# Kernel optimization log

Hardware: AMD Instinct MI355X
Metric: run time of the kernel (lower is better)

Reference implementation:

```python
import jax, jax.numpy as jnp
import numpy as np

B, C, H, W = 8, 512, 64, 64
S = 64
STD = 0.001  # torch init.normal_(weight, std=0.001)


def setup_inputs() -> dict:
    key = jax.random.key(0)
    ks = jax.random.split(key, 7)
    return {
        "queries": jax.random.normal(ks[0], (B, C, H, W), dtype=jnp.float32),
        "k": jax.random.normal(ks[1], (B, C, H, W), dtype=jnp.float32),
        "v": jax.random.normal(ks[2], (B, C, H, W), dtype=jnp.float32),
        "Wq": jax.random.normal(ks[3], (S, C), dtype=jnp.float32) * STD,
        "Wk": jax.random.normal(ks[4], (S, C), dtype=jnp.float32) * STD,
        "Wv": jax.random.normal(ks[5], (S, C), dtype=jnp.float32) * STD,
        "Wl": jax.random.normal(ks[6], (C, S), dtype=jnp.float32) * STD,
    }


def _branch(A, Bp, Cp, Wl):
    # A,Bp,Cp: [h,w,b,S] projected tensors
    m = jnp.einsum('hwbs,hwbt->hwst', A, Bp)          # [h,w,S,S]
    m = jax.nn.softmax(m, axis=1)                      # softmax over w (dim=1, as in torch)
    o = jnp.einsum('hwst,hwbt->hwsb', m, Cp)           # [h,w,S,b]
    o = o / jnp.sum(o, axis=2, keepdims=True)          # normalize over S
    o = jnp.einsum('hwsb,cs->hwbc', o, Wl)             # transpose + Linear(S->C)
    return jnp.transpose(o, (2, 3, 0, 1))              # [b,c,h,w]


def reference(queries, k, v, Wq, Wk, Wv, Wl):
    q = jnp.transpose(queries, (2, 3, 0, 1))  # [h,w,b,c]
    kk = jnp.transpose(k, (2, 3, 0, 1))
    vv = jnp.transpose(v, (2, 3, 0, 1))
    aq = jnp.einsum('hwbc,sc->hwbs', q, Wq)   # [h,w,b,S]
    ak = jnp.einsum('hwbc,sc->hwbs', kk, Wk)
    av = jnp.einsum('hwbc,sc->hwbs', vv, Wv)
    out_q = _branch(aq, ak, av, Wl)
    out_k = _branch(ak, av, aq, Wl)
    out_v = _branch(av, aq, ak, Wl)
    return jnp.concatenate((out_q, out_k, out_v), axis=0)  # [3b,c,h,w]
```

## Files before the change

### kernel.cpp

```cpp
#include <hip/hip_runtime.h>
#include <hip/hip_bf16.h>

#define HW 4096
#define CCH 512
#define SDIM 64
#define BDIM 8

typedef __attribute__((ext_vector_type(8))) short short8;
typedef __attribute__((ext_vector_type(4))) float f32x4;

static __device__ __forceinline__ ushort f2bf(float f) {
  __hip_bfloat16 h = __float2bfloat16(f);
  return *reinterpret_cast<ushort*>(&h);
}
static __device__ __forceinline__ float bf2f(ushort u) {
  union { unsigned int u32; float f; } c;
  c.u32 = ((unsigned int)u) << 16;
  return c.f;
}
static __device__ __forceinline__ ushort trunc_bf(float f, float* rem) {
  union { float f; unsigned int u; } a; a.f = f;
  union { float f; unsigned int u; } h; h.u = a.u & 0xFFFF0000u;
  *rem = f - h.f;
  return (ushort)(a.u >> 16);
}
static __device__ __forceinline__ ushort rne_bf(float f) {
  union { float f; unsigned int u; } a; a.f = f;
  return (ushort)((a.u + 0x8000u) >> 16);
}

__global__ __launch_bounds__(256) void prep_kernel(const float* __restrict__ Wq,
                                                   const float* __restrict__ Wk,
                                                   const float* __restrict__ Wv,
                                                   const float* __restrict__ Wl,
                                                   ushort* __restrict__ whi,
                                                   ushort* __restrict__ wmid,
                                                   ushort* __restrict__ wlo,
                                                   ushort* __restrict__ wlhi,
                                                   ushort* __restrict__ wllo) {
  const int idx = blockIdx.x * 1024 + threadIdx.x * 4;
  if (blockIdx.y == 3) {
    float4 f = *reinterpret_cast<const float4*>(&Wl[idx]);
    ushort4 h, l;
    float r;
    h.x = trunc_bf(f.x, &r); l.x = rne_bf(r);
    h.y = trunc_bf(f.y, &r); l.y = rne_bf(r);
    h.z = trunc_bf(f.z, &r); l.z = rne_bf(r);
    h.w = trunc_bf(f.w, &r); l.w = rne_bf(r);
    *reinterpret_cast<ushort4*>(&wlhi[idx]) = h;
    *reinterpret_cast<ushort4*>(&wllo[idx]) = l;
    return;
  }
  const float* W = blockIdx.y == 0 ? Wq : (blockIdx.y == 1 ? Wk : Wv);
  float4 f = *reinterpret_cast<const float4*>(&W[idx]);
  ushort4 h, m, l;
  float r, r2;
  h.x = f2bf(f.x); r = f.x - bf2f(h.x); m.x = f2bf(r); r2 = r - bf2f(m.x); l.x = f2bf(r2);
  h.y = f2bf(f.y); r = f.y - bf2f(h.y); m.y = f2bf(r); r2 = r - bf2f(m.y); l.y = f2bf(r2);
  h.z = f2bf(f.z); r = f.z - bf2f(h.z); m.z = f2bf(r); r2 = r - bf2f(m.z); l.z = f2bf(r2);
  h.w = f2bf(f.w); r = f.w - bf2f(h.w); m.w = f2bf(r); r2 = r - bf2f(m.w); l.w = f2bf(r2);
  const size_t o = (size_t)blockIdx.y * (SDIM * CCH) + idx;
  *reinterpret_cast<ushort4*>(&whi[o])  = h;
  *reinterpret_cast<ushort4*>(&wmid[o]) = m;
  *reinterpret_cast<ushort4*>(&wlo[o])  = l;
}

__global__ __launch_bounds__(256) void proj_mfma_kernel(const float* __restrict__ q,
                                                        const float* __restrict__ k,
                                                        const float* __restrict__ v,
                                                        const ushort* __restrict__ whi,
                                                        const ushort* __restrict__ wmid,
                                                        const ushort* __restrict__ wlo,
                                                        float* __restrict__ ap) {
  __shared__ float Xs[64 * 128];
  const int mt = blockIdx.x;
  const int b = blockIdx.y;
  const int br = blockIdx.z;
  const float* x = br == 0 ? q : (br == 1 ? k : v);
  const ushort* wh = whi + (size_t)br * SDIM * CCH;
  const ushort* wm = wmid + (size_t)br * SDIM * CCH;
  const ushort* wl = wlo + (size_t)br * SDIM * CCH;
  float* apo = ap + (size_t)br * HW * 512;
  const int hw0 = mt * 128;
  const int tid = threadIdx.x;
  const int l = tid & 63;
  const int wstrip = (tid >> 6) * 32;
  const int row16 = l & 15;
  const int kgrp = l >> 4;

  f32x4 acc_hi[2][4] = {};
  f32x4 acc_co[2][4] = {};

  for (int c0 = 0; c0 < CCH; c0 += 64) {
    __syncthreads();
#pragma unroll
    for (int it = 0; it < 8; ++it) {
      const int fidx = (it * 256 + tid) * 4;
      const int cc = fidx >> 7;
      const int hwi = fidx & 127;
      const int hws = hwi ^ (((cc >> 3) & 1) << 4);
      *reinterpret_cast<float4*>(&Xs[cc * 128 + hws]) =
          *reinterpret_cast<const float4*>(&x[(size_t)(b * CCH + c0 + cc) * HW + hw0 + hwi]);
    }
    __syncthreads();
#pragma unroll
    for (int ks = 0; ks < 2; ++ks) {
      short8 bh[4], bm[4], bl[4];
#pragma unroll
      for (int nf = 0; nf < 4; ++nf) {
        const size_t off = (size_t)(nf * 16 + row16) * CCH + c0 + ks * 32 + kgrp * 8;
        bh[nf] = *reinterpret_cast<const short8*>(&wh[off]);
        bm[nf] = *reinterpret_cast<const short8*>(&wm[off]);
        bl[nf] = *reinterpret_cast<const short8*>(&wl[off]);
      }
#pragma unroll
      for (int mf = 0; mf < 2; ++mf) {
        const int rowA = wstrip + mf * 16 + row16;
        short8 ah, am, al;
        {
          ushort th[8], tm[8], tl[8];
#pragma unroll
          for (int i = 0; i < 8; ++i) {
            const int c = ks * 32 + kgrp * 8 + i;
            const float f = Xs[c * 128 + (rowA ^ (((c >> 3) & 1) << 4))];
            float r, r2;
            th[i] = trunc_bf(f, &r);
            tm[i] = trunc_bf(r, &r2);
            tl[i] = rne_bf(r2);
          }
          ah = *reinterpret_cast<const short8*>(th);
          am = *reinterpret_cast<const short8*>(tm);
          al = *reinterpret_cast<const short8*>(tl);
        }
#pragma unroll
        for (int nf = 0; nf < 4; ++nf) {
          acc_hi[mf][nf] = __builtin_amdgcn_mfma_f32_16x16x32_bf16(ah, bh[nf], acc_hi[mf][nf], 0, 0, 0);
          acc_co[mf][nf] = __builtin_amdgcn_mfma_f32_16x16x32_bf16(ah, bm[nf], acc_co[mf][nf], 0, 0, 0);
          acc_co[mf][nf] = __builtin_amdgcn_mfma_f32_16x16x32_bf16(am, bh[nf], acc_co[mf][nf], 0, 0, 0);
          acc_co[mf][nf] = __builtin_amdgcn_mfma_f32_16x16x32_bf16(am, bm[nf], acc_co[mf][nf], 0, 0, 0);
          acc_co[mf][nf] = __builtin_amdgcn_mfma_f32_16x16x32_bf16(ah, bl[nf], acc_co[mf][nf], 0, 0, 0);
          acc_co[mf][nf] = __builtin_amdgcn_mfma_f32_16x16x32_bf16(al, bh[nf], acc_co[mf][nf], 0, 0, 0);
          acc_co[mf][nf] = __builtin_amdgcn_mfma_f32_16x16x32_bf16(am, bl[nf], acc_co[mf][nf], 0, 0, 0);
          acc_co[mf][nf] = __builtin_amdgcn_mfma_f32_16x16x32_bf16(al, bm[nf], acc_co[mf][nf], 0, 0, 0);
        }
      }
    }
  }
#pragma unroll
  for (int mf = 0; mf < 2; ++mf)
#pragma unroll
    for (int nf = 0; nf < 4; ++nf)
#pragma unroll
      for (int r = 0; r < 4; ++r) {
        const int m = hw0 + wstrip + mf * 16 + kgrp * 4 + r;
        apo[(size_t)m * 512 + b * 64 + nf * 16 + row16] = acc_hi[mf][nf][r] + acc_co[mf][nf][r];
      }
}

__global__ __launch_bounds__(512) void denom_kernel(const float* __restrict__ ap,
                                                    float* __restrict__ rD) {
  __shared__ float As[8 * 16];
  __shared__ float Bs[8 * 64];
  const int h = blockIdx.x, br = blockIdx.y, sq = blockIdx.z;
  const float* A  = ap + ((size_t)br * HW + (size_t)h * 64) * (BDIM * SDIM);
  const float* Bp = ap + ((size_t)((br + 1) % 3) * HW + (size_t)h * 64) * (BDIM * SDIM);
  const int tid = threadIdx.x;
  const int t = tid & 63;
  const int sg = tid >> 6;
  float D[2] = {};
  for (int w = 0; w < 64; ++w) {
    __syncthreads();
    if (tid < 128) As[tid] = A[w * 512 + (tid >> 4) * 64 + sq * 16 + (tid & 15)];
    Bs[tid] = Bp[w * 512 + tid];
    __syncthreads();
    float bv[8];
#pragma unroll
    for (int b = 0; b < 8; ++b) bv[b] = Bs[b * 64 + t];
#pragma unroll
    for (int j = 0; j < 2; ++j) {
      const int sl = sg * 2 + j;
      float m = 0.f;
#pragma unroll
      for (int b = 0; b < 8; ++b) m = fmaf(As[b * 16 + sl], bv[b], m);
      D[j] += __expf(m);
    }
  }
#pragma unroll
  for (int j = 0; j < 2; ++j)
    rD[((size_t)(br * 64 + h) * 64 + sq * 16 + sg * 2 + j) * 64 + t] = 1.0f / D[j];
}

__global__ __launch_bounds__(256) void attn_kernel(const float* __restrict__ ap,
                                                   const float* __restrict__ rD,
                                                   float* __restrict__ on) {
  __shared__ float As[8 * 64], Bs[8 * 64], Cs[8 * 64];
  __shared__ float Ms[64 * 68];
  const int wc = blockIdx.x, h = blockIdx.y, br = blockIdx.z;
  const float* A  = ap + ((size_t)br * HW + h * 64) * 512;
  const float* Bp = ap + ((size_t)((br + 1) % 3) * HW + h * 64) * 512;
  const float* Cp = ap + ((size_t)((br + 2) % 3) * HW + h * 64) * 512;
  const float* rDp = rD + (size_t)(br * 64 + h) * 4096;
  const int tid = threadIdx.x;
  for (int w = wc * 8; w < wc * 8 + 8; ++w) {
    __syncthreads();
#pragma unroll
    for (int it = 0; it < 2; ++it) {
      int idx = it * 256 + tid;
      As[idx] = A[w * 512 + idx];
      Bs[idx] = Bp[w * 512 + idx];
      Cs[idx] = Cp[w * 512 + idx];
    }
    __syncthreads();
    {
      const int t = tid & 63, sg = tid >> 6;
      float bv[8];
#pragma unroll
      for (int b = 0; b < 8; ++b) bv[b] = Bs[b * 64 + t];
#pragma unroll
      for (int j = 0; j < 16; ++j) {
        int s = sg * 16 + j;
        float m = 0.f;
#pragma unroll
        for (int b = 0; b < 8; ++b) m = fmaf(As[b * 64 + s], bv[b], m);
        Ms[s * 68 + t] = __expf(m) * rDp[s * 64 + t];
      }
    }
    __syncthreads();
    const int s2 = tid & 63, bq = tid >> 6;
    float o0 = 0.f, o1 = 0.f;
#pragma unroll
    for (int tt = 0; tt < 64; tt += 4) {
      float4 mv = *reinterpret_cast<const float4*>(&Ms[s2 * 68 + tt]);
      float4 c0 = *reinterpret_cast<const float4*>(&Cs[bq * 64 + tt]);
      float4 c1 = *reinterpret_cast<const float4*>(&Cs[(bq + 4) * 64 + tt]);
      o0 = fmaf(mv.w, c0.w, fmaf(mv.z, c0.z, fmaf(mv.y, c0.y, fmaf(mv.x, c0.x, o0))));
      o1 = fmaf(mv.w, c1.w, fmaf(mv.z, c1.z, fmaf(mv.y, c1.y, fmaf(mv.x, c1.x, o1))));
    }
    float n0 = o0, n1 = o1;
#pragma unroll
    for (int off = 32; off > 0; off >>= 1) {
      n0 += __shfl_xor(n0, off);
      n1 += __shfl_xor(n1, off);
    }
    const float r0 = 1.0f / n0, r1 = 1.0f / n1;
    const size_t ob = ((size_t)br * HW + h * 64 + w) * 512;
    on[ob + (size_t)bq * 64 + s2] = o0 * r0;
    on[ob + (size_t)(bq + 4) * 64 + s2] = o1 * r1;
  }
}

__global__ __launch_bounds__(256) void out_kernel(const float* __restrict__ on,
                                                  const ushort* __restrict__ wlhi,
                                                  const ushort* __restrict__ wllo,
                                                  float* __restrict__ out) {
  __shared__ float Os[128 * 68];
  const int hwt = blockIdx.x;
  const int brb = blockIdx.y;
  const int br = brb >> 3, b = brb & 7;
  const int hw0 = hwt * 128;
  const int tid = threadIdx.x;
  const int l = tid & 63;
  const int wv = tid >> 6;
  const int l15 = l & 15;
  const int kgrp = l >> 4;

  {
    const int row = tid >> 4;
    const int s4 = (tid & 15) * 4;
#pragma unroll
    for (int it = 0; it < 8; ++it) {
      const int r = row + it * 16;
      *reinterpret_cast<float4*>(&Os[r * 68 + s4]) =
          *reinterpret_cast<const float4*>(&on[((size_t)(br * HW + hw0 + r) * 8 + b) * 64 + s4]);
    }
  }
  __syncthreads();

  short8 onh[2][2], onl[2][2];
#pragma unroll
  for (int nf = 0; nf < 2; ++nf)
#pragma unroll
    for (int ks = 0; ks < 2; ++ks) {
      const int row = wv * 32 + nf * 16 + l15;
      const float* p = &Os[row * 68 + ks * 32 + kgrp * 8];
      ushort th[8], tl[8];
#pragma unroll
      for (int i = 0; i < 8; ++i) {
        float r;
        th[i] = trunc_bf(p[i], &r);
        tl[i] = rne_bf(r);
      }
      onh[nf][ks] = *reinterpret_cast<const short8*>(th);
      onl[nf][ks] = *reinterpret_cast<const short8*>(tl);
    }

  for (int mf = 0; mf < 32; ++mf) {
    f32x4 acc[2] = {};
#pragma unroll
    for (int ks = 0; ks < 2; ++ks) {
      const size_t woff = (size_t)(mf * 16 + l15) * 64 + ks * 32 + kgrp * 8;
      const short8 wh8 = *reinterpret_cast<const short8*>(&wlhi[woff]);
      const short8 wl8 = *reinterpret_cast<const short8*>(&wllo[woff]);
#pragma unroll
      for (int nf = 0; nf < 2; ++nf) {
        acc[nf] = __builtin_amdgcn_mfma_f32_16x16x32_bf16(wh8, onh[nf][ks], acc[nf], 0, 0, 0);
        acc[nf] = __builtin_amdgcn_mfma_f32_16x16x32_bf16(wh8, onl[nf][ks], acc[nf], 0, 0, 0);
        acc[nf] = __builtin_amdgcn_mfma_f32_16x16x32_bf16(wl8, onh[nf][ks], acc[nf], 0, 0, 0);
      }
    }
#pragma unroll
    for (int nf = 0; nf < 2; ++nf)
#pragma unroll
      for (int r = 0; r < 4; ++r) {
        const int cc = mf * 16 + kgrp * 4 + r;
        out[(size_t)(brb * 512 + cc) * HW + hw0 + wv * 32 + nf * 16 + l15] = acc[nf][r];
      }
  }
}

extern "C" void kernel_launch(void* const* d_in, const int* in_sizes, int n_in,
                              void* d_out, int out_size, void* d_ws, size_t ws_size,
                              hipStream_t stream) {
  const float* q  = (const float*)d_in[0];
  const float* k  = (const float*)d_in[1];
  const float* v  = (const float*)d_in[2];
  const float* Wq = (const float*)d_in[3];
  const float* Wk = (const float*)d_in[4];
  const float* Wv = (const float*)d_in[5];
  const float* Wl = (const float*)d_in[6];
  float* out = (float*)d_out;

  float* ap = (float*)d_ws;
  float* rD = ap + (size_t)3 * HW * 512;
  float* on = rD + (size_t)3 * 64 * 64 * 64;
  ushort* whi  = (ushort*)rD;
  ushort* wmid = whi + (size_t)3 * SDIM * CCH;
  ushort* wlo  = wmid + (size_t)3 * SDIM * CCH;
  ushort* wlhi = (ushort*)(on + (size_t)3 * HW * 512);
  ushort* wllo = wlhi + (size_t)SDIM * CCH;

  prep_kernel<<<dim3(32, 4), 256, 0, stream>>>(Wq, Wk, Wv, Wl, whi, wmid, wlo, wlhi, wllo);
  proj_mfma_kernel<<<dim3(32, 8, 3), 256, 0, stream>>>(q, k, v, whi, wmid, wlo, ap);
  denom_kernel<<<dim3(64, 3, 4), 512, 0, stream>>>(ap, rD);
  attn_kernel<<<dim3(8, 64, 3), 256, 0, stream>>>(ap, rD, on);
  out_kernel<<<dim3(32, 24), 256, 0, stream>>>(on, wlhi, wllo, out);
}
```

Measured before the change: 283.0 us.

## Double-buffer projection loads via global_load_lds and transpose attention Ms layout

```diff
diff --git a/kernel.cpp b/kernel.cpp
--- a/kernel.cpp
+++ b/kernel.cpp
@@ -27,6 +27,11 @@
 static __device__ __forceinline__ ushort rne_bf(float f) {
   union { float f; unsigned int u; } a; a.f = f;
   return (ushort)((a.u + 0x8000u) >> 16);
+}
+static __device__ __forceinline__ void gll16(const float* g, float* lds_base) {
+  __builtin_amdgcn_global_load_lds(
+      (const __attribute__((address_space(1))) unsigned int*)g,
+      (__attribute__((address_space(3))) unsigned int*)lds_base, 16, 0, 0);
 }
 
 __global__ __launch_bounds__(256) void prep_kernel(const float* __restrict__ Wq,
@@ -72,7 +77,7 @@
                                                         const ushort* __restrict__ wmid,
                                                         const ushort* __restrict__ wlo,
                                                         float* __restrict__ ap) {
-  __shared__ float Xs[64 * 128];
+  __shared__ float Xs[2 * 32 * 128];
   const int mt = blockIdx.x;
   const int b = blockIdx.y;
   const int br = blockIdx.z;
@@ -84,68 +89,86 @@
   const int hw0 = mt * 128;
   const int tid = threadIdx.x;
   const int l = tid & 63;
-  const int wstrip = (tid >> 6) * 32;
+  const int wid = tid >> 6;
+  const int wstrip = wid * 32;
   const int row16 = l & 15;
   const int kgrp = l >> 4;
+  const float* xcol = x + (size_t)b * CCH * HW + hw0;
+  const int rbase = 8 * wid;
+  const int rsub = l >> 5;
+  const int hws = (l & 31) * 4;
 
   f32x4 acc_hi[2][4] = {};
   f32x4 acc_co[2][4] = {};
 
-  for (int c0 = 0; c0 < CCH; c0 += 64) {
-    __syncthreads();
-#pragma unroll
-    for (int it = 0; it < 8; ++it) {
-      const int fidx = (it * 256 + tid) * 4;
-      const int cc = fidx >> 7;
-      const int hwi = fidx & 127;
-      const int hws = hwi ^ (((cc >> 3) & 1) << 4);
-      *reinterpret_cast<float4*>(&Xs[cc * 128 + hws]) =
-          *reinterpret_cast<const float4*>(&x[(size_t)(b * CCH + c0 + cc) * HW + hw0 + hwi]);
-    }
-    __syncthreads();
-#pragma unroll
-    for (int ks = 0; ks < 2; ++ks) {
-      short8 bh[4], bm[4], bl[4];
+#pragma unroll
+  for (int j = 0; j < 4; ++j) {
+    const int r = rbase + 2 * j + rsub;
+    gll16(xcol + (size_t)r * HW + hws, &Xs[(rbase + 2 * j) * 128]);
+  }
+
+  for (int ci = 0; ci < 16; ++ci) {
+    short8 bh[4], bm[4], bl[4];
+#pragma unroll
+    for (int nf = 0; nf < 4; ++nf) {
+      const size_t off = (size_t)(nf * 16 + row16) * CCH + ci * 32 + kgrp * 8;
+      bh[nf] = *reinterpret_cast<const short8*>(&wh[off]);
+      bm[nf] = *reinterpret_cast<const short8*>(&wm[off]);
+      bl[nf] = *reinterpret_cast<const short8*>(&wl[off]);
+    }
+    __builtin_amdgcn_sched_barrier(0);
+    if (ci < 15) {
+      float* dst = &Xs[((ci + 1) & 1) * 4096];
+#pragma unroll
+      for (int j = 0; j < 4; ++j) {
+        const int r = rbase + 2 * j + rsub;
+        gll16(xcol + (size_t)((ci + 1) * 32 + r) * HW + hws, dst + (rbase + 2 * j) * 128);
+      }
+      __builtin_amdgcn_sched_barrier(0);
+      asm volatile("s_waitcnt vmcnt(4)" ::: "memory");
+    } else {
+      asm volatile("s_waitcnt vmcnt(0)" ::: "memory");
+    }
+    __builtin_amdgcn_sched_barrier(0);
+    __builtin_amdgcn_s_barrier();
+    __builtin_amdgcn_sched_barrier(0);
+
+    const float* lw = &Xs[(ci & 1) * 4096];
+#pragma unroll
+    for (int mf = 0; mf < 2; ++mf) {
+      const int rowA = wstrip + mf * 16 + row16;
+      short8 ah, am, al;
+      {
+        ushort th[8], tm[8], tl[8];
+#pragma unroll
+        for (int i = 0; i < 8; ++i) {
+          const float f = lw[(kgrp * 8 + i) * 128 + rowA];
+          float r, r2;
+          th[i] = trunc_bf(f, &r);
+          tm[i] = trunc_bf(r, &r2);
+          tl[i] = rne_bf(r2);
+        }
+        ah = *reinterpret_cast<const short8*>(th);
+        am = *reinterpret_cast<const short8*>(tm);
+        al = *reinterpret_cast<const short8*>(tl);
+      }
 #pragma unroll
       for (int nf = 0; nf < 4; ++nf) {
-        const size_t off = (size_t)(nf * 16 + row16) * CCH + c0 + ks * 32 + kgrp * 8;
-        bh[nf] = *reinterpret_cast<const short8*>(&wh[off]);
-        bm[nf] = *reinterpret_cast<const short8*>(&wm[off]);
-        bl[nf] = *reinterpret_cast<const short8*>(&wl[off]);
-      }
-#pragma unroll
-      for (int mf = 0; mf < 2; ++mf) {
-        const int rowA = wstrip + mf * 16 + row16;
-        short8 ah, am, al;
-        {
-          ushort th[8], tm[8], tl[8];
-#pragma unroll
-          for (int i = 0; i < 8; ++i) {
-            const int c = ks * 32 + kgrp * 8 + i;
-            const float f = Xs[c * 128 + (rowA ^ (((c >> 3) & 1) << 4))];
-            float r, r2;
-            th[i] = trunc_bf(f, &r);
-            tm[i] = trunc_bf(r, &r2);
-            tl[i] = rne_bf(r2);
-          }
-          ah = *reinterpret_cast<const short8*>(th);
-          am = *reinterpret_cast<const short8*>(tm);
-          al = *reinterpret_cast<const short8*>(tl);
-        }
-#pragma unroll
-        for (int nf = 0; nf < 4; ++nf) {
-          acc_hi[mf][nf] = __builtin_amdgcn_mfma_f32_16x16x32_bf16(ah, bh[nf], acc_hi[mf][nf], 0, 0, 0);
-          acc_co[mf][nf] = __builtin_amdgcn_mfma_f32_16x16x32_bf16(ah, bm[nf], acc_co[mf][nf], 0, 0, 0);
-          acc_co[mf][nf] = __builtin_amdgcn_mfma_f32_16x16x32_bf16(am, bh[nf], acc_co[mf][nf], 0, 0, 0);
-          acc_co[mf][nf] = __builtin_amdgcn_mfma_f32_16x16x32_bf16(am, bm[nf], acc_co[mf][nf], 0, 0, 0);
-          acc_co[mf][nf] = __builtin_amdgcn_mfma_f32_16x16x32_bf16(ah, bl[nf], acc_co[mf][nf], 0, 0, 0);
-          acc_co[mf][nf] = __builtin_amdgcn_mfma_f32_16x16x32_bf16(al, bh[nf], acc_co[mf][nf], 0, 0, 0);
-          acc_co[mf][nf] = __builtin_amdgcn_mfma_f32_16x16x32_bf16(am, bl[nf], acc_co[mf][nf], 0, 0, 0);
-          acc_co[mf][nf] = __builtin_amdgcn_mfma_f32_16x16x32_bf16(al, bm[nf], acc_co[mf][nf], 0, 0, 0);
-        }
-      }
-    }
-  }
+        acc_hi[mf][nf] = __builtin_amdgcn_mfma_f32_16x16x32_bf16(ah, bh[nf], acc_hi[mf][nf], 0, 0, 0);
+        acc_co[mf][nf] = __builtin_amdgcn_mfma_f32_16x16x32_bf16(ah, bm[nf], acc_co[mf][nf], 0, 0, 0);
+        acc_co[mf][nf] = __builtin_amdgcn_mfma_f32_16x16x32_bf16(am, bh[nf], acc_co[mf][nf], 0, 0, 0);
+        acc_co[mf][nf] = __builtin_amdgcn_mfma_f32_16x16x32_bf16(am, bm[nf], acc_co[mf][nf], 0, 0, 0);
+        acc_co[mf][nf] = __builtin_amdgcn_mfma_f32_16x16x32_bf16(ah, bl[nf], acc_co[mf][nf], 0, 0, 0);
+        acc_co[mf][nf] = __builtin_amdgcn_mfma_f32_16x16x32_bf16(al, bh[nf], acc_co[mf][nf], 0, 0, 0);
+        acc_co[mf][nf] = __builtin_amdgcn_mfma_f32_16x16x32_bf16(am, bl[nf], acc_co[mf][nf], 0, 0, 0);
+        acc_co[mf][nf] = __builtin_amdgcn_mfma_f32_16x16x32_bf16(al, bm[nf], acc_co[mf][nf], 0, 0, 0);
+      }
+    }
+    __builtin_amdgcn_sched_barrier(0);
+    __builtin_amdgcn_s_barrier();
+    __builtin_amdgcn_sched_barrier(0);
+  }
+
 #pragma unroll
   for (int mf = 0; mf < 2; ++mf)
 #pragma unroll
@@ -194,7 +217,7 @@
                                                    const float* __restrict__ rD,
                                                    float* __restrict__ on) {
   __shared__ float As[8 * 64], Bs[8 * 64], Cs[8 * 64];
-  __shared__ float Ms[64 * 68];
+  __shared__ float Ms[64 * 65];
   const int wc = blockIdx.x, h = blockIdx.y, br = blockIdx.z;
   const float* A  = ap + ((size_t)br * HW + h * 64) * 512;
   const float* Bp = ap + ((size_t)((br + 1) % 3) * HW + h * 64) * 512;
@@ -222,7 +245,7 @@
         float m = 0.f;
 #pragma unroll
         for (int b = 0; b < 8; ++b) m = fmaf(As[b * 64 + s], bv[b], m);
-        Ms[s * 68 + t] = __expf(m) * rDp[s * 64 + t];
+        Ms[t * 65 + s] = __expf(m) * rDp[s * 64 + t];
       }
     }
     __syncthreads();
@@ -230,11 +253,14 @@
     float o0 = 0.f, o1 = 0.f;
 #pragma unroll
     for (int tt = 0; tt < 64; tt += 4) {
-      float4 mv = *reinterpret_cast<const float4*>(&Ms[s2 * 68 + tt]);
+      const float m0 = Ms[(tt + 0) * 65 + s2];
+      const float m1 = Ms[(tt + 1) * 65 + s2];
+      const float m2 = Ms[(tt + 2) * 65 + s2];
+      const float m3 = Ms[(tt + 3) * 65 + s2];
       float4 c0 = *reinterpret_cast<const float4*>(&Cs[bq * 64 + tt]);
       float4 c1 = *reinterpret_cast<const float4*>(&Cs[(bq + 4) * 64 + tt]);
-      o0 = fmaf(mv.w, c0.w, fmaf(mv.z, c0.z, fmaf(mv.y, c0.y, fmaf(mv.x, c0.x, o0))));
-      o1 = fmaf(mv.w, c1.w, fmaf(mv.z, c1.z, fmaf(mv.y, c1.y, fmaf(mv.x, c1.x, o1))));
+      o0 = fmaf(m3, c0.w, fmaf(m2, c0.z, fmaf(m1, c0.y, fmaf(m0, c0.x, o0))));
+      o1 = fmaf(m3, c1.w, fmaf(m2, c1.z, fmaf(m1, c1.y, fmaf(m0, c1.x, o1))));
     }
     float n0 = o0, n1 = o1;
 #pragma unroll
```

After: 280.6 us. About the same (-0.8%).
